# Optimization experiments

Hardware: AMD Instinct MI355X
Metric: run time of the kernel (lower is better)

The kernel has to match this reference:

```python
import jax, jax.numpy as jnp
import numpy as np

N_NODES = 100000
N_EDGES = 1600000
NFEAT = 256
NCLASS = 2


def setup_inputs() -> dict:
    key = jax.random.key(0)
    ks = jax.random.split(key, 16)
    x = jax.random.normal(ks[0], (N_NODES, NFEAT), dtype=jnp.float32)
    row = jax.random.randint(ks[1], (N_EDGES,), 0, N_NODES, dtype=jnp.int64) if jax.config.jax_enable_x64 else jax.random.randint(ks[1], (N_EDGES,), 0, N_NODES, dtype=jnp.int32)
    col = jax.random.randint(ks[2], (N_EDGES,), 0, N_NODES, dtype=row.dtype)
    edge_val = jax.random.uniform(ks[3], (N_EDGES,), dtype=jnp.float32)

    def unif(k, shape, fan_out):
        stdv = 1.0 / np.sqrt(fan_out)
        return jax.random.uniform(k, shape, dtype=jnp.float32, minval=-stdv, maxval=stdv)

    W1 = unif(ks[4], (NFEAT, 32), 32); b1 = unif(ks[5], (32,), 32)
    W2 = unif(ks[6], (32, 48), 48);   b2 = unif(ks[7], (48,), 48)
    W3 = unif(ks[8], (48, 64), 64);   b3 = unif(ks[9], (64,), 64)
    fc1_W = unif(ks[10], (64, 32), 64); fc1_b = unif(ks[11], (32,), 64)
    fc2_W = unif(ks[12], (32, NCLASS), 32); fc2_b = unif(ks[13], (NCLASS,), 32)
    return {"x": x, "row": row, "col": col, "edge_val": edge_val,
            "W1": W1, "b1": b1, "W2": W2, "b2": b2, "W3": W3, "b3": b3,
            "fc1_W": fc1_W, "fc1_b": fc1_b, "fc2_W": fc2_W, "fc2_b": fc2_b}


def _spmm(row, col, val, dense):
    # out[i] = sum_{e: row[e]==i} val[e] * dense[col[e]]   (COO sparse @ dense)
    gathered = dense[col] * val[:, None]          # [E, F]
    return jax.ops.segment_sum(gathered, row, num_segments=N_NODES)


def _gc_layer(x, row, col, val, W, b):
    support = x @ W                               # dense mm  [N, out]
    return _spmm(row, col, val, support) + b      # spmm + bias


def reference(x, row, col, edge_val, W1, b1, W2, b2, W3, b3, fc1_W, fc1_b, fc2_W, fc2_b):
    # eval mode: dropout is identity
    h = jax.nn.relu(_gc_layer(x, row, col, edge_val, W1, b1))   # [N, 32]
    h = jax.nn.relu(_gc_layer(h, row, col, edge_val, W2, b2))   # [N, 48]
    h = jax.nn.relu(_gc_layer(h, row, col, edge_val, W3, b3))   # [N, 64]
    y = jnp.mean(h, axis=0)                                     # [64] global mean pool
    y = jax.nn.relu(y @ fc1_W + fc1_b)                          # [32]
    y = jax.nn.softmax(y @ fc2_W + fc2_b, axis=0)               # [nclass]
    return y
```

## Files before the change

### kernel.cpp

```cpp
#include <hip/hip_runtime.h>
#include <hip/hip_bf16.h>

#define N_NODES 100000
#define N_EDGES 1600000

#define NT 391
#define NB1 128
#define CHUNK ((N_EDGES + NB1 - 1) / NB1)
#define ROWS3 80
#define GRID3 (N_NODES / ROWS3)

__device__ __forceinline__ unsigned char f2q(float f) {
    return (unsigned char)(__builtin_amdgcn_cvt_pk_fp8_f32(f, f, 0, false) & 0xFF);
}
__device__ __forceinline__ unsigned pack4_fp8(float a0, float a1, float a2, float a3) {
    int r = __builtin_amdgcn_cvt_pk_fp8_f32(a0, a1, 0, false);
    r = __builtin_amdgcn_cvt_pk_fp8_f32(a2, a3, r, true);
    return (unsigned)r;
}
#define CVT(u, s) __builtin_amdgcn_cvt_f32_fp8((u), (s))

#define ACC16(A, U, V)                                                              \
    A[0]  += (V) * CVT((U).x, 0); A[1]  += (V) * CVT((U).x, 1);                     \
    A[2]  += (V) * CVT((U).x, 2); A[3]  += (V) * CVT((U).x, 3);                     \
    A[4]  += (V) * CVT((U).y, 0); A[5]  += (V) * CVT((U).y, 1);                     \
    A[6]  += (V) * CVT((U).y, 2); A[7]  += (V) * CVT((U).y, 3);                     \
    A[8]  += (V) * CVT((U).z, 0); A[9]  += (V) * CVT((U).z, 1);                     \
    A[10] += (V) * CVT((U).z, 2); A[11] += (V) * CVT((U).z, 3);                     \
    A[12] += (V) * CVT((U).w, 0); A[13] += (V) * CVT((U).w, 1);                     \
    A[14] += (V) * CVT((U).w, 2); A[15] += (V) * CVT((U).w, 3);


__global__ __launch_bounds__(256) void k_phist(const int* __restrict__ row, int* __restrict__ blkhist) {
    __shared__ int h[NT];
    int b = blockIdx.x, t = threadIdx.x;
    for (int i = t; i < NT; i += 256) h[i] = 0;
    __syncthreads();
    int s = b * CHUNK, e = min(s + CHUNK, N_EDGES);
    for (int i = s + t; i < e; i += 256) atomicAdd(&h[row[i] >> 8], 1);
    __syncthreads();
    for (int i = t; i < NT; i += 256) blkhist[i * NB1 + b] = h[i];
}

__global__ __launch_bounds__(128) void k_bscan1(int* __restrict__ blkhist, int* __restrict__ cnt) {
    __shared__ int s[128];
    int j = blockIdx.x, t = threadIdx.x;
    int v = blkhist[j * NB1 + t];
    s[t] = v;
    __syncthreads();
    #pragma unroll
    for (int st = 1; st < 128; st <<= 1) {
        int u = (t >= st) ? s[t - st] : 0;
        __syncthreads();
        s[t] += u;
        __syncthreads();
    }
    blkhist[j * NB1 + t] = s[t] - v;
    if (t == 127) cnt[j] = s[127];
}

__global__ __launch_bounds__(512) void k_bscan2(const int* __restrict__ cnt, int* __restrict__ base,
                                                int* __restrict__ row_ptr) {
    __shared__ int s[512];
    int j = threadIdx.x;
    int v = (j < NT) ? cnt[j] : 0;
    s[j] = v;
    __syncthreads();
    for (int st = 1; st < 512; st <<= 1) {
        int u = (j >= st) ? s[j - st] : 0;
        __syncthreads();
        s[j] += u;
        __syncthreads();
    }
    if (j < NT) base[j] = s[j] - v;
    if (j == 0) row_ptr[N_NODES] = N_EDGES;
}

__global__ __launch_bounds__(256) void k_pscatter(const int* __restrict__ row, const int* __restrict__ col,
                                                  const float* __restrict__ val,
                                                  const int* __restrict__ blkhist, const int* __restrict__ base,
                                                  int2* __restrict__ part) {
    __shared__ int cur[NT];
    int b = blockIdx.x, t = threadIdx.x;
    for (int i = t; i < NT; i += 256) cur[i] = blkhist[i * NB1 + b] + base[i];
    __syncthreads();
    int s = b * CHUNK, e = min(s + CHUNK, N_EDGES);
    for (int i = s + t; i < e; i += 256) {
        int r = row[i];
        int j = r >> 8;
        int p = atomicAdd(&cur[j], 1);
        part[p] = make_int2(((r & 255) << 24) | col[i], __float_as_int(val[i]));
    }
}

__global__ __launch_bounds__(256) void k_sort(const int2* __restrict__ part, const int* __restrict__ cnt,
                                              const int* __restrict__ base, int* __restrict__ row_ptr,
                                              unsigned* __restrict__ csr) {
    __shared__ int hist[256];
    __shared__ int cur[256];
    int b = blockIdx.x, t = threadIdx.x;
    int n = cnt[b];
    int bb = base[b];
    const int2* sl = part + bb;
    hist[t] = 0;
    __syncthreads();
    for (int i = t; i < n; i += 256) atomicAdd(&hist[((unsigned)sl[i].x) >> 24], 1);
    __syncthreads();
    int v = hist[t];
    for (int st = 1; st < 256; st <<= 1) {
        int u = (t >= st) ? hist[t - st] : 0;
        __syncthreads();
        hist[t] += u;
        __syncthreads();
    }
    cur[t] = hist[t] - v;
    int grow = b * 256 + t;
    if (grow < N_NODES) row_ptr[grow] = bb + cur[t];
    __syncthreads();
    for (int i = t; i < n; i += 256) {
        int2 e = sl[i];
        int rl = ((unsigned)e.x) >> 24;
        int p = atomicAdd(&cur[rl], 1);
        unsigned c = (unsigned)(e.x & 0xFFFFFF);
        float vf = __int_as_float(e.y);
        int q = __float2int_rn(vf * 32768.0f);
        if (q > 32767) q = 32767;
        csr[bb + p] = (c << 15) | (unsigned)q;
    }
}

__global__ __launch_bounds__(256) void k_gemm1(const float* __restrict__ x, const float* __restrict__ W,
                                               unsigned char* __restrict__ out) {
    __shared__ float xs[64][68];
    __shared__ __align__(16) float wc[64 * 32];
    int tid = threadIdx.x;
    int bn = blockIdx.x * 64;
    int nl = tid >> 3;
    int o4 = (tid & 7) * 4;
    float acc[2][4] = {};
    for (int kc = 0; kc < 4; ++kc) {
        int k0 = kc * 64;
        #pragma unroll
        for (int i = 0; i < 4; ++i) {
            int idx = i * 256 + tid;
            int n = idx >> 4;
            int k4 = (idx & 15) * 4;
            float4 v = make_float4(0.f, 0.f, 0.f, 0.f);
            if (bn + n < N_NODES)
                v = *reinterpret_cast<const float4*>(&x[(size_t)(bn + n) * 256 + k0 + k4]);
            *reinterpret_cast<float4*>(&xs[n][k4]) = v;
        }
        #pragma unroll
        for (int i = 0; i < 2; ++i) {
            int idx = i * 256 + tid;
            reinterpret_cast<float4*>(wc)[idx] =
                reinterpret_cast<const float4*>(W + (size_t)k0 * 32)[idx];
        }
        __syncthreads();
        #pragma unroll 8
        for (int k = 0; k < 64; ++k) {
            float a0 = xs[nl][k];
            float a1 = xs[nl + 32][k];
            float4 w = *reinterpret_cast<const float4*>(&wc[k * 32 + o4]);
            acc[0][0] += a0 * w.x; acc[0][1] += a0 * w.y; acc[0][2] += a0 * w.z; acc[0][3] += a0 * w.w;
            acc[1][0] += a1 * w.x; acc[1][1] += a1 * w.y; acc[1][2] += a1 * w.z; acc[1][3] += a1 * w.w;
        }
        __syncthreads();
    }
    #pragma unroll
    for (int i = 0; i < 2; ++i) {
        int n = bn + nl + 32 * i;
        if (n < N_NODES) {
            unsigned r = pack4_fp8(acc[i][0], acc[i][1], acc[i][2], acc[i][3]);
            *reinterpret_cast<unsigned*>(&out[(size_t)n * 32 + o4]) = r;
        }
    }
}

__global__ __launch_bounds__(256, 8) void k_spmm1(const int* __restrict__ rp, const unsigned* __restrict__ csr,
                                                  const unsigned char* __restrict__ sup,
                                                  const float* __restrict__ bias,
                                                  unsigned char* __restrict__ out) {
    int gid = blockIdx.x * 256 + threadIdx.x;
    int n = gid >> 1;
    if (n >= N_NODES) return;
    int f16 = (gid & 1) * 16;
    int e0 = rp[n], e1 = rp[n + 1];
    float a[16] = {};
    int e = e0;
    if ((e & 1) && e < e1) {
        unsigned ent = csr[e];
        float v = (float)(ent & 0x7FFF);
        uint4 u = *reinterpret_cast<const uint4*>(&sup[(size_t)(ent >> 15) * 32 + f16]);
        ACC16(a, u, v)
        ++e;
    }
    for (; e + 1 < e1; e += 2) {
        uint2 p = *reinterpret_cast<const uint2*>(&csr[e]);
        uint4 u = *reinterpret_cast<const uint4*>(&sup[(size_t)(p.x >> 15) * 32 + f16]);
        uint4 w = *reinterpret_cast<const uint4*>(&sup[(size_t)(p.y >> 15) * 32 + f16]);
        float v0 = (float)(p.x & 0x7FFF), v1 = (float)(p.y & 0x7FFF);
        ACC16(a, u, v0)
        ACC16(a, w, v1)
    }
    if (e < e1) {
        unsigned ent = csr[e];
        float v = (float)(ent & 0x7FFF);
        uint4 u = *reinterpret_cast<const uint4*>(&sup[(size_t)(ent >> 15) * 32 + f16]);
        ACC16(a, u, v)
    }
    const float sc = 1.0f / 32768.0f;
    uint4 r;
    r.x = pack4_fp8(fmaxf(a[0] * sc + bias[f16 + 0], 0.f),  fmaxf(a[1] * sc + bias[f16 + 1], 0.f),
                    fmaxf(a[2] * sc + bias[f16 + 2], 0.f),  fmaxf(a[3] * sc + bias[f16 + 3], 0.f));
    r.y = pack4_fp8(fmaxf(a[4] * sc + bias[f16 + 4], 0.f),  fmaxf(a[5] * sc + bias[f16 + 5], 0.f),
                    fmaxf(a[6] * sc + bias[f16 + 6], 0.f),  fmaxf(a[7] * sc + bias[f16 + 7], 0.f));
    r.z = pack4_fp8(fmaxf(a[8] * sc + bias[f16 + 8], 0.f),  fmaxf(a[9] * sc + bias[f16 + 9], 0.f),
                    fmaxf(a[10] * sc + bias[f16 + 10], 0.f), fmaxf(a[11] * sc + bias[f16 + 11], 0.f));
    r.w = pack4_fp8(fmaxf(a[12] * sc + bias[f16 + 12], 0.f), fmaxf(a[13] * sc + bias[f16 + 13], 0.f),
                    fmaxf(a[14] * sc + bias[f16 + 14], 0.f), fmaxf(a[15] * sc + bias[f16 + 15], 0.f));
    *reinterpret_cast<uint4*>(&out[(size_t)n * 32 + f16]) = r;
}

__global__ __launch_bounds__(256, 8) void k_l2fused(const int* __restrict__ rp, const unsigned* __restrict__ csr,
                                                    const unsigned char* __restrict__ h1,
                                                    const float* __restrict__ W2, const float* __restrict__ b2,
                                                    unsigned char* __restrict__ h2) {
    __shared__ float w2s[32 * 48];
    __shared__ float b2s[48];
    __shared__ float g2s[128][33];
    int tid = threadIdx.x;
    for (int i = tid; i < 32 * 48; i += 256) w2s[i] = W2[i];
    if (tid < 48) b2s[tid] = b2[tid];
    int n0 = blockIdx.x * 128;
    int grp = tid >> 1;
    int f16 = (tid & 1) * 16;
    int n = n0 + grp;
    if (n < N_NODES) {
        int e0 = rp[n], e1 = rp[n + 1];
        float a[16] = {};
        int e = e0;
        if ((e & 1) && e < e1) {
            unsigned ent = csr[e];
            float v = (float)(ent & 0x7FFF);
            uint4 u = *reinterpret_cast<const uint4*>(&h1[(size_t)(ent >> 15) * 32 + f16]);
            ACC16(a, u, v)
            ++e;
        }
        for (; e + 1 < e1; e += 2) {
            uint2 p = *reinterpret_cast<const uint2*>(&csr[e]);
            uint4 u = *reinterpret_cast<const uint4*>(&h1[(size_t)(p.x >> 15) * 32 + f16]);
            uint4 w = *reinterpret_cast<const uint4*>(&h1[(size_t)(p.y >> 15) * 32 + f16]);
            float v0 = (float)(p.x & 0x7FFF), v1 = (float)(p.y & 0x7FFF);
            ACC16(a, u, v0)
            ACC16(a, w, v1)
        }
        if (e < e1) {
            unsigned ent = csr[e];
            float v = (float)(ent & 0x7FFF);
            uint4 u = *reinterpret_cast<const uint4*>(&h1[(size_t)(ent >> 15) * 32 + f16]);
            ACC16(a, u, v)
        }
        const float sc = 1.0f / 32768.0f;
        #pragma unroll
        for (int j = 0; j < 16; ++j) g2s[grp][f16 + j] = a[j] * sc;
    }
    __syncthreads();
    #pragma unroll
    for (int pp = 0; pp < 24; ++pp) {
        int idx = pp * 256 + tid;
        int r = idx / 48;
        int m = idx - 48 * r;
        if (n0 + r < N_NODES) {
            float a = b2s[m];
            const float* g = g2s[r];
            #pragma unroll
            for (int k = 0; k < 32; ++k) a += g[k] * w2s[k * 48 + m];
            h2[(size_t)(n0 + r) * 48 + m] = f2q(fmaxf(a, 0.f));
        }
    }
}

__global__ __launch_bounds__(256, 8) void k_l3fused(const int* __restrict__ rp, const unsigned* __restrict__ csr,
                                                    const unsigned char* __restrict__ h2,
                                                    const float* __restrict__ W3, const float* __restrict__ b3,
                                                    float* __restrict__ poolpart) {
    __shared__ float w3s[48 * 64];
    __shared__ float b3s[64];
    __shared__ float g3s[ROWS3][49];
    __shared__ float red[256];
    int tid = threadIdx.x;
    for (int i = tid; i < 48 * 64; i += 256) w3s[i] = W3[i];
    if (tid < 64) b3s[tid] = b3[tid];
    int grp = tid / 3;
    int f16 = (tid - grp * 3) * 16;
    int m = tid & 63;
    const float sc = 1.0f / 32768.0f;
    if (tid < 240) {
        int n = blockIdx.x * ROWS3 + grp;
        int e0 = rp[n], e1 = rp[n + 1];
        float a[16] = {};
        int e = e0;
        if ((e & 1) && e < e1) {
            unsigned ent = csr[e];
            float v = (float)(ent & 0x7FFF);
            uint4 u = *reinterpret_cast<const uint4*>(&h2[(size_t)(ent >> 15) * 48 + f16]);
            ACC16(a, u, v)
            ++e;
        }
        for (; e + 1 < e1; e += 2) {
            uint2 p = *reinterpret_cast<const uint2*>(&csr[e]);
            uint4 u = *reinterpret_cast<const uint4*>(&h2[(size_t)(p.x >> 15) * 48 + f16]);
            uint4 w = *reinterpret_cast<const uint4*>(&h2[(size_t)(p.y >> 15) * 48 + f16]);
            float v0 = (float)(p.x & 0x7FFF), v1 = (float)(p.y & 0x7FFF);
            ACC16(a, u, v0)
            ACC16(a, w, v1)
        }
        if (e < e1) {
            unsigned ent = csr[e];
            float v = (float)(ent & 0x7FFF);
            uint4 u = *reinterpret_cast<const uint4*>(&h2[(size_t)(ent >> 15) * 48 + f16]);
            ACC16(a, u, v)
        }
        #pragma unroll
        for (int j = 0; j < 16; ++j) g3s[grp][f16 + j] = a[j] * sc;
    }
    __syncthreads();
    float poolacc = 0.f;
    #pragma unroll
    for (int pp = 0; pp < 20; ++pp) {
        int r = 4 * pp + (tid >> 6);
        float a = b3s[m];
        const float* gg = g3s[r];
        #pragma unroll
        for (int k = 0; k < 48; ++k) a += gg[k] * w3s[k * 64 + m];
        poolacc += fmaxf(a, 0.f);
    }
    red[tid] = poolacc;
    __syncthreads();
    if (tid < 64) {
        float s = red[tid] + red[tid + 64] + red[tid + 128] + red[tid + 192];
        poolpart[(size_t)blockIdx.x * 64 + tid] = s;
    }
}

__global__ __launch_bounds__(256) void k_preduce(const float* __restrict__ poolpart,
                                                 float* __restrict__ pool) {
    __shared__ float red[256];
    int b = blockIdx.x, t = threadIdx.x;
    float s = 0.f;
    for (int j = t; j < GRID3; j += 256) s += poolpart[(size_t)j * 64 + b];
    red[t] = s;
    __syncthreads();
    for (int st = 128; st > 0; st >>= 1) {
        if (t < st) red[t] += red[t + st];
        __syncthreads();
    }
    if (t == 0) pool[b] = red[0];
}

__global__ __launch_bounds__(64) void k_head(const float* __restrict__ pool,
                                             const float* __restrict__ fc1W, const float* __restrict__ fc1b,
                                             const float* __restrict__ fc2W, const float* __restrict__ fc2b,
                                             float* __restrict__ out) {
    __shared__ float pl[64];
    __shared__ float z[32];
    __shared__ float lg[2];
    int t = threadIdx.x;
    pl[t] = pool[t] * (1.0f / (float)N_NODES);
    __syncthreads();
    if (t < 32) {
        float a = fc1b[t];
        #pragma unroll
        for (int o = 0; o < 64; ++o) a += pl[o] * fc1W[o * 32 + t];
        z[t] = fmaxf(a, 0.f);
    }
    __syncthreads();
    if (t < 2) {
        float l = fc2b[t];
        #pragma unroll
        for (int j = 0; j < 32; ++j) l += z[j] * fc2W[j * 2 + t];
        lg[t] = l;
    }
    __syncthreads();
    if (t == 0) {
        float mx = fmaxf(lg[0], lg[1]);
        float e0 = __expf(lg[0] - mx), e1 = __expf(lg[1] - mx);
        float ss = e0 + e1;
        out[0] = e0 / ss;
        out[1] = e1 / ss;
    }
}


extern "C" void kernel_launch(void* const* d_in, const int* in_sizes, int n_in,
                              void* d_out, int out_size, void* d_ws, size_t ws_size,
                              hipStream_t stream) {
    const float* x    = (const float*)d_in[0];
    const int*   row  = (const int*)d_in[1];
    const int*   col  = (const int*)d_in[2];
    const float* val  = (const float*)d_in[3];
    const float* W1   = (const float*)d_in[4];
    const float* b1   = (const float*)d_in[5];
    const float* W2   = (const float*)d_in[6];
    const float* b2   = (const float*)d_in[7];
    const float* W3   = (const float*)d_in[8];
    const float* b3   = (const float*)d_in[9];
    const float* fc1W = (const float*)d_in[10];
    const float* fc1b = (const float*)d_in[11];
    const float* fc2W = (const float*)d_in[12];
    const float* fc2b = (const float*)d_in[13];
    float* out = (float*)d_out;

    char* wsb = (char*)d_ws;
    size_t off = 0;
    auto alloc = [&](size_t bytes) {
        void* p = wsb + off;
        off += (bytes + 255) / 256 * 256;
        return p;
    };
    int*      blkhist  = (int*)alloc((size_t)NT * NB1 * 4);
    int*      base     = (int*)alloc((size_t)NT * 4);
    int*      cnt      = (int*)alloc((size_t)NT * 4);
    int*      row_ptr  = (int*)alloc((size_t)(N_NODES + 1) * 4);
    int2*     part     = (int2*)alloc((size_t)N_EDGES * 8);
    unsigned* csr      = (unsigned*)alloc((size_t)N_EDGES * 4);
    unsigned char* sup = (unsigned char*)alloc((size_t)N_NODES * 32);
    unsigned char* h1  = (unsigned char*)alloc((size_t)N_NODES * 32);
    unsigned char* h2  = (unsigned char*)alloc((size_t)N_NODES * 48);
    float* poolpart    = (float*)alloc((size_t)GRID3 * 64 * 4);
    float* pool        = (float*)alloc(64 * 4);

    k_phist<<<NB1, 256, 0, stream>>>(row, blkhist);
    k_bscan1<<<NT, 128, 0, stream>>>(blkhist, cnt);
    k_bscan2<<<1, 512, 0, stream>>>(cnt, base, row_ptr);
    k_pscatter<<<NB1, 256, 0, stream>>>(row, col, val, blkhist, base, part);
    k_sort<<<NT, 256, 0, stream>>>(part, cnt, base, row_ptr, csr);

    k_gemm1<<<(N_NODES + 63) / 64, 256, 0, stream>>>(x, W1, sup);
    k_spmm1<<<(N_NODES * 2 + 255) / 256, 256, 0, stream>>>(row_ptr, csr, sup, b1, h1);
    k_l2fused<<<(N_NODES + 127) / 128, 256, 0, stream>>>(row_ptr, csr, h1, W2, b2, h2);
    k_l3fused<<<GRID3, 256, 0, stream>>>(row_ptr, csr, h2, W3, b3, poolpart);
    k_preduce<<<64, 256, 0, stream>>>(poolpart, pool);
    k_head<<<1, 64, 0, stream>>>(pool, fc1W, fc1b, fc2W, fc2b, out);
}
```

Baseline: 214.1 us.

## Merge gemm1 with row histogram launch and unroll SpMM edge loops by four

The first dense GEMM and the row histogram of the CSR build now run as one launch, with extra blocks taking the histogram role, so the two independent stages overlap and one launch is dropped. The SpMM edge loops in all three layers now load four CSR entries at once and issue four gathers per iteration, aligning to a 4-entry boundary first, to raise memory-level parallelism. Launch-bounds occupancy hints are lowered to 6 and 5 waves to give the wider loops more registers, at the cost of fewer resident waves.

```diff
diff --git a/kernel.cpp b/kernel.cpp
--- a/kernel.cpp
+++ b/kernel.cpp
@@ -9,6 +9,7 @@
 #define CHUNK ((N_EDGES + NB1 - 1) / NB1)
 #define ROWS3 80
 #define GRID3 (N_NODES / ROWS3)
+#define GB1 ((N_NODES + 63) / 64)
 
 __device__ __forceinline__ unsigned char f2q(float f) {
     return (unsigned char)(__builtin_amdgcn_cvt_pk_fp8_f32(f, f, 0, false) & 0xFF);
@@ -30,17 +31,67 @@
     A[12] += (V) * CVT((U).w, 0); A[13] += (V) * CVT((U).w, 1);                     \
     A[14] += (V) * CVT((U).w, 2); A[15] += (V) * CVT((U).w, 3);
 
-
-__global__ __launch_bounds__(256) void k_phist(const int* __restrict__ row, int* __restrict__ blkhist) {
-    __shared__ int h[NT];
-    int b = blockIdx.x, t = threadIdx.x;
-    for (int i = t; i < NT; i += 256) h[i] = 0;
-    __syncthreads();
-    int s = b * CHUNK, e = min(s + CHUNK, N_EDGES);
-    for (int i = s + t; i < e; i += 256) atomicAdd(&h[row[i] >> 8], 1);
-    __syncthreads();
-    for (int i = t; i < NT; i += 256) blkhist[i * NB1 + b] = h[i];
-}
+__global__ __launch_bounds__(256) void k_gemm1_phist(const float* __restrict__ x, const float* __restrict__ W,
+                                                     unsigned char* __restrict__ out,
+                                                     const int* __restrict__ row, int* __restrict__ blkhist) {
+    __shared__ __align__(16) char smem[64 * 68 * 4 + 64 * 32 * 4];
+    int tid = threadIdx.x;
+    if (blockIdx.x >= GB1) {
+        int* h = (int*)smem;
+        int b = blockIdx.x - GB1;
+        for (int i = tid; i < NT; i += 256) h[i] = 0;
+        __syncthreads();
+        int s = b * CHUNK, e = min(s + CHUNK, N_EDGES);
+        for (int i = s + tid; i < e; i += 256) atomicAdd(&h[row[i] >> 8], 1);
+        __syncthreads();
+        for (int i = tid; i < NT; i += 256) blkhist[i * NB1 + b] = h[i];
+        return;
+    }
+    float (*xs)[68] = (float(*)[68])smem;
+    float* wc = (float*)(smem + 64 * 68 * 4);
+    int bn = blockIdx.x * 64;
+    int nl = tid >> 3;
+    int o4 = (tid & 7) * 4;
+    float acc[2][4] = {};
+    for (int kc = 0; kc < 4; ++kc) {
+        int k0 = kc * 64;
+        #pragma unroll
+        for (int i = 0; i < 4; ++i) {
+            int idx = i * 256 + tid;
+            int n = idx >> 4;
+            int k4 = (idx & 15) * 4;
+            float4 v = make_float4(0.f, 0.f, 0.f, 0.f);
+            if (bn + n < N_NODES)
+                v = *reinterpret_cast<const float4*>(&x[(size_t)(bn + n) * 256 + k0 + k4]);
+            *reinterpret_cast<float4*>(&xs[n][k4]) = v;
+        }
+        #pragma unroll
+        for (int i = 0; i < 2; ++i) {
+            int idx = i * 256 + tid;
+            reinterpret_cast<float4*>(wc)[idx] =
+                reinterpret_cast<const float4*>(W + (size_t)k0 * 32)[idx];
+        }
+        __syncthreads();
+        #pragma unroll 8
+        for (int k = 0; k < 64; ++k) {
+            float a0 = xs[nl][k];
+            float a1 = xs[nl + 32][k];
+            float4 w = *reinterpret_cast<const float4*>(&wc[k * 32 + o4]);
+            acc[0][0] += a0 * w.x; acc[0][1] += a0 * w.y; acc[0][2] += a0 * w.z; acc[0][3] += a0 * w.w;
+            acc[1][0] += a1 * w.x; acc[1][1] += a1 * w.y; acc[1][2] += a1 * w.z; acc[1][3] += a1 * w.w;
+        }
+        __syncthreads();
+    }
+    #pragma unroll
+    for (int i = 0; i < 2; ++i) {
+        int n = bn + nl + 32 * i;
+        if (n < N_NODES) {
+            unsigned r = pack4_fp8(acc[i][0], acc[i][1], acc[i][2], acc[i][3]);
+            *reinterpret_cast<unsigned*>(&out[(size_t)n * 32 + o4]) = r;
+        }
+    }
+}
+
 
 __global__ __launch_bounds__(128) void k_bscan1(int* __restrict__ blkhist, int* __restrict__ cnt) {
     __shared__ int s[128];
@@ -129,55 +180,7 @@
     }
 }
 
-__global__ __launch_bounds__(256) void k_gemm1(const float* __restrict__ x, const float* __restrict__ W,
-                                               unsigned char* __restrict__ out) {
-    __shared__ float xs[64][68];
-    __shared__ __align__(16) float wc[64 * 32];
-    int tid = threadIdx.x;
-    int bn = blockIdx.x * 64;
-    int nl = tid >> 3;
-    int o4 = (tid & 7) * 4;
-    float acc[2][4] = {};
-    for (int kc = 0; kc < 4; ++kc) {
-        int k0 = kc * 64;
-        #pragma unroll
-        for (int i = 0; i < 4; ++i) {
-            int idx = i * 256 + tid;
-            int n = idx >> 4;
-            int k4 = (idx & 15) * 4;
-            float4 v = make_float4(0.f, 0.f, 0.f, 0.f);
-            if (bn + n < N_NODES)
-                v = *reinterpret_cast<const float4*>(&x[(size_t)(bn + n) * 256 + k0 + k4]);
-            *reinterpret_cast<float4*>(&xs[n][k4]) = v;
-        }
-        #pragma unroll
-        for (int i = 0; i < 2; ++i) {
-            int idx = i * 256 + tid;
-            reinterpret_cast<float4*>(wc)[idx] =
-                reinterpret_cast<const float4*>(W + (size_t)k0 * 32)[idx];
-        }
-        __syncthreads();
-        #pragma unroll 8
-        for (int k = 0; k < 64; ++k) {
-            float a0 = xs[nl][k];
-            float a1 = xs[nl + 32][k];
-            float4 w = *reinterpret_cast<const float4*>(&wc[k * 32 + o4]);
-            acc[0][0] += a0 * w.x; acc[0][1] += a0 * w.y; acc[0][2] += a0 * w.z; acc[0][3] += a0 * w.w;
-            acc[1][0] += a1 * w.x; acc[1][1] += a1 * w.y; acc[1][2] += a1 * w.z; acc[1][3] += a1 * w.w;
-        }
-        __syncthreads();
-    }
-    #pragma unroll
-    for (int i = 0; i < 2; ++i) {
-        int n = bn + nl + 32 * i;
-        if (n < N_NODES) {
-            unsigned r = pack4_fp8(acc[i][0], acc[i][1], acc[i][2], acc[i][3]);
-            *reinterpret_cast<unsigned*>(&out[(size_t)n * 32 + o4]) = r;
-        }
-    }
-}
-
-__global__ __launch_bounds__(256, 8) void k_spmm1(const int* __restrict__ rp, const unsigned* __restrict__ csr,
+__global__ __launch_bounds__(256, 6) void k_spmm1(const int* __restrict__ rp, const unsigned* __restrict__ csr,
                                                   const unsigned char* __restrict__ sup,
                                                   const float* __restrict__ bias,
                                                   unsigned char* __restrict__ out) {
@@ -188,22 +191,26 @@
     int e0 = rp[n], e1 = rp[n + 1];
     float a[16] = {};
     int e = e0;
-    if ((e & 1) && e < e1) {
+    for (; (e & 3) && e < e1; ++e) {
         unsigned ent = csr[e];
         float v = (float)(ent & 0x7FFF);
         uint4 u = *reinterpret_cast<const uint4*>(&sup[(size_t)(ent >> 15) * 32 + f16]);
         ACC16(a, u, v)
-        ++e;
-    }
-    for (; e + 1 < e1; e += 2) {
-        uint2 p = *reinterpret_cast<const uint2*>(&csr[e]);
-        uint4 u = *reinterpret_cast<const uint4*>(&sup[(size_t)(p.x >> 15) * 32 + f16]);
-        uint4 w = *reinterpret_cast<const uint4*>(&sup[(size_t)(p.y >> 15) * 32 + f16]);
+    }
+    for (; e + 3 < e1; e += 4) {
+        uint4 p = *reinterpret_cast<const uint4*>(&csr[e]);
+        uint4 u0 = *reinterpret_cast<const uint4*>(&sup[(size_t)(p.x >> 15) * 32 + f16]);
+        uint4 u1 = *reinterpret_cast<const uint4*>(&sup[(size_t)(p.y >> 15) * 32 + f16]);
+        uint4 u2 = *reinterpret_cast<const uint4*>(&sup[(size_t)(p.z >> 15) * 32 + f16]);
+        uint4 u3 = *reinterpret_cast<const uint4*>(&sup[(size_t)(p.w >> 15) * 32 + f16]);
         float v0 = (float)(p.x & 0x7FFF), v1 = (float)(p.y & 0x7FFF);
-        ACC16(a, u, v0)
-        ACC16(a, w, v1)
-    }
-    if (e < e1) {
+        float v2 = (float)(p.z & 0x7FFF), v3 = (float)(p.w & 0x7FFF);
+        ACC16(a, u0, v0)
+        ACC16(a, u1, v1)
+        ACC16(a, u2, v2)
+        ACC16(a, u3, v3)
+    }
+    for (; e < e1; ++e) {
         unsigned ent = csr[e];
         float v = (float)(ent & 0x7FFF);
         uint4 u = *reinterpret_cast<const uint4*>(&sup[(size_t)(ent >> 15) * 32 + f16]);
@@ -222,7 +229,7 @@
     *reinterpret_cast<uint4*>(&out[(size_t)n * 32 + f16]) = r;
 }
 
-__global__ __launch_bounds__(256, 8) void k_l2fused(const int* __restrict__ rp, const unsigned* __restrict__ csr,
+__global__ __launch_bounds__(256, 6) void k_l2fused(const int* __restrict__ rp, const unsigned* __restrict__ csr,
                                                     const unsigned char* __restrict__ h1,
                                                     const float* __restrict__ W2, const float* __restrict__ b2,
                                                     unsigned char* __restrict__ h2) {
@@ -240,22 +247,26 @@
         int e0 = rp[n], e1 = rp[n + 1];
         float a[16] = {};
         int e = e0;
-        if ((e & 1) && e < e1) {
+        for (; (e & 3) && e < e1; ++e) {
             unsigned ent = csr[e];
             float v = (float)(ent & 0x7FFF);
             uint4 u = *reinterpret_cast<const uint4*>(&h1[(size_t)(ent >> 15) * 32 + f16]);
             ACC16(a, u, v)
-            ++e;
-        }
-        for (; e + 1 < e1; e += 2) {
-            uint2 p = *reinterpret_cast<const uint2*>(&csr[e]);
-            uint4 u = *reinterpret_cast<const uint4*>(&h1[(size_t)(p.x >> 15) * 32 + f16]);
-            uint4 w = *reinterpret_cast<const uint4*>(&h1[(size_t)(p.y >> 15) * 32 + f16]);
+        }
+        for (; e + 3 < e1; e += 4) {
+            uint4 p = *reinterpret_cast<const uint4*>(&csr[e]);
+            uint4 u0 = *reinterpret_cast<const uint4*>(&h1[(size_t)(p.x >> 15) * 32 + f16]);
+            uint4 u1 = *reinterpret_cast<const uint4*>(&h1[(size_t)(p.y >> 15) * 32 + f16]);
+            uint4 u2 = *reinterpret_cast<const uint4*>(&h1[(size_t)(p.z >> 15) * 32 + f16]);
+            uint4 u3 = *reinterpret_cast<const uint4*>(&h1[(size_t)(p.w >> 15) * 32 + f16]);
             float v0 = (float)(p.x & 0x7FFF), v1 = (float)(p.y & 0x7FFF);
-            ACC16(a, u, v0)
-            ACC16(a, w, v1)
-        }
-        if (e < e1) {
+            float v2 = (float)(p.z & 0x7FFF), v3 = (float)(p.w & 0x7FFF);
+            ACC16(a, u0, v0)
+            ACC16(a, u1, v1)
+            ACC16(a, u2, v2)
+            ACC16(a, u3, v3)
+        }
+        for (; e < e1; ++e) {
             unsigned ent = csr[e];
             float v = (float)(ent & 0x7FFF);
             uint4 u = *reinterpret_cast<const uint4*>(&h1[(size_t)(ent >> 15) * 32 + f16]);
@@ -281,7 +292,7 @@
     }
 }
 
-__global__ __launch_bounds__(256, 8) void k_l3fused(const int* __restrict__ rp, const unsigned* __restrict__ csr,
+__global__ __launch_bounds__(256, 5) void k_l3fused(const int* __restrict__ rp, const unsigned* __restrict__ csr,
                                                     const unsigned char* __restrict__ h2,
                                                     const float* __restrict__ W3, const float* __restrict__ b3,
                                                     float* __restrict__ poolpart) {
@@ -301,22 +312,26 @@
         int e0 = rp[n], e1 = rp[n + 1];
         float a[16] = {};
         int e = e0;
-        if ((e & 1) && e < e1) {
+        for (; (e & 3) && e < e1; ++e) {
             unsigned ent = csr[e];
             float v = (float)(ent & 0x7FFF);
             uint4 u = *reinterpret_cast<const uint4*>(&h2[(size_t)(ent >> 15) * 48 + f16]);
             ACC16(a, u, v)
-            ++e;
-        }
-        for (; e + 1 < e1; e += 2) {
-            uint2 p = *reinterpret_cast<const uint2*>(&csr[e]);
-            uint4 u = *reinterpret_cast<const uint4*>(&h2[(size_t)(p.x >> 15) * 48 + f16]);
-            uint4 w = *reinterpret_cast<const uint4*>(&h2[(size_t)(p.y >> 15) * 48 + f16]);
+        }
+        for (; e + 3 < e1; e += 4) {
+            uint4 p = *reinterpret_cast<const uint4*>(&csr[e]);
+            uint4 u0 = *reinterpret_cast<const uint4*>(&h2[(size_t)(p.x >> 15) * 48 + f16]);
+            uint4 u1 = *reinterpret_cast<const uint4*>(&h2[(size_t)(p.y >> 15) * 48 + f16]);
+            uint4 u2 = *reinterpret_cast<const uint4*>(&h2[(size_t)(p.z >> 15) * 48 + f16]);
+            uint4 u3 = *reinterpret_cast<const uint4*>(&h2[(size_t)(p.w >> 15) * 48 + f16]);
             float v0 = (float)(p.x & 0x7FFF), v1 = (float)(p.y & 0x7FFF);
-            ACC16(a, u, v0)
-            ACC16(a, w, v1)
-        }
-        if (e < e1) {
+            float v2 = (float)(p.z & 0x7FFF), v3 = (float)(p.w & 0x7FFF);
+            ACC16(a, u0, v0)
+            ACC16(a, u1, v1)
+            ACC16(a, u2, v2)
+            ACC16(a, u3, v3)
+        }
+        for (; e < e1; ++e) {
             unsigned ent = csr[e];
             float v = (float)(ent & 0x7FFF);
             uint4 u = *reinterpret_cast<const uint4*>(&h2[(size_t)(ent >> 15) * 48 + f16]);
@@ -431,13 +446,12 @@
     float* poolpart    = (float*)alloc((size_t)GRID3 * 64 * 4);
     float* pool        = (float*)alloc(64 * 4);
 
-    k_phist<<<NB1, 256, 0, stream>>>(row, blkhist);
+    k_gemm1_phist<<<GB1 + NB1, 256, 0, stream>>>(x, W1, sup, row, blkhist);
     k_bscan1<<<NT, 128, 0, stream>>>(blkhist, cnt);
     k_bscan2<<<1, 512, 0, stream>>>(cnt, base, row_ptr);
     k_pscatter<<<NB1, 256, 0, stream>>>(row, col, val, blkhist, base, part);
     k_sort<<<NT, 256, 0, stream>>>(part, cnt, base, row_ptr, csr);
 
-    k_gemm1<<<(N_NODES + 63) / 64, 256, 0, stream>>>(x, W1, sup);
     k_spmm1<<<(N_NODES * 2 + 255) / 256, 256, 0, stream>>>(row_ptr, csr, sup, b1, h1);
     k_l2fused<<<(N_NODES + 127) / 128, 256, 0, stream>>>(row_ptr, csr, h1, W2, b2, h2);
     k_l3fused<<<GRID3, 256, 0, stream>>>(row_ptr, csr, h2, W3, b3, poolpart);
```

Measured after the change: 220.5 us. +3.0%, slower.
